# Optimization experiments

Measured on AMD Instinct MI355X. Metric: run time of the kernel, lower is better.

## Reference

```python
import jax, jax.numpy as jnp
import numpy as np

B, T, D = 4, 4096, 1024


def setup_inputs() -> dict:
    key = jax.random.key(0)
    ks = jax.random.split(key, 7)
    s_in = 1.0 / np.sqrt(D)
    return {
        "x": jax.random.normal(ks[0], (B, T, D), dtype=jnp.float32),
        "W_in": jax.random.uniform(ks[1], (D, 2 * D), jnp.float32, -s_in, s_in),
        "b_in": jax.random.uniform(ks[2], (2 * D,), jnp.float32, -s_in, s_in),
        "A": jax.random.normal(ks[3], (D,), dtype=jnp.float32),
        "C": jax.random.normal(ks[4], (D,), dtype=jnp.float32),
        "W_out": jax.random.uniform(ks[5], (D, D), jnp.float32, -s_in, s_in),
        "b_out": jax.random.uniform(ks[6], (D,), jnp.float32, -s_in, s_in),
    }


def _ssm(v, A, C):
    # diagonal linear recurrence: h_t = sigmoid(A) * h_{t-1} + v_t ; y_t = C * h_t
    decay = jax.nn.sigmoid(A)  # (D,)
    vT = jnp.swapaxes(v, 0, 1)  # (T, B, D)

    def step(h, vt):
        h = decay * h + vt
        return h, h

    h0 = jnp.zeros(vT.shape[1:], dtype=v.dtype)
    _, hs = jax.lax.scan(step, h0, vT)  # (T, B, D)
    return jnp.swapaxes(hs, 0, 1) * C  # (B, T, D)


def reference(x, W_in, b_in, A, C, W_out, b_out):
    proj = x @ W_in + b_in  # (B, T, 2D)
    v, gate = jnp.split(proj, 2, axis=-1)
    gate = jax.nn.sigmoid(gate)
    y = gate * _ssm(v, A, C)
    return y @ W_out + b_out
```

## Files before the change

kernel.cpp:

```cpp
#include <hip/hip_runtime.h>
#include <math.h>

#define BDIM 4
#define TDIM 4096
#define DDIM 1024
#define MDIM (BDIM * TDIM)

#define NC  64
#define LCH 64
static_assert(NC * LCH == TDIM, "chunking");

typedef __attribute__((ext_vector_type(8))) short short8;
typedef __attribute__((ext_vector_type(4))) float f32x4;

__device__ __forceinline__ unsigned short f2bf(float f) {
  unsigned int u = __float_as_uint(f);
  unsigned int r = (u + 0x7fffu + ((u >> 16) & 1u)) >> 16;
  return (unsigned short)r;
}
__device__ __forceinline__ float bf2f(unsigned short h) {
  return __uint_as_float(((unsigned int)h) << 16);
}
__device__ __forceinline__ float sigmoidf_(float x) {
  return 1.0f / (1.0f + expf(-x));
}

__global__ __launch_bounds__(256) void prep_x_kernel(const float* __restrict__ x,
                                                     unsigned short* __restrict__ xh,
                                                     int n4) {
  int i = blockIdx.x * 256 + threadIdx.x;
  if (i >= n4) return;
  float4 f = ((const float4*)x)[i];
  ushort4 h;
  h.x = f2bf(f.x);
  h.y = f2bf(f.y);
  h.z = f2bf(f.z);
  h.w = f2bf(f.w);
  ((ushort4*)xh)[i] = h;
}

__global__ __launch_bounds__(256) void wprep_kernel(const float* __restrict__ in,
                                                    unsigned short* __restrict__ oh,
                                                    int K, int N) {
  __shared__ float t[64][65];
  int n0 = blockIdx.x * 64;
  int k0 = blockIdx.y * 64;
#pragma unroll
  for (int i = 0; i < 16; ++i) {
    int idx = i * 256 + threadIdx.x;
    int r = idx >> 6, c = idx & 63;
    t[r][c] = in[(size_t)(k0 + r) * N + (n0 + c)];
  }
  __syncthreads();
#pragma unroll
  for (int i = 0; i < 16; ++i) {
    int idx = i * 256 + threadIdx.x;
    int rn = idx >> 6, ck = idx & 63;
    oh[(size_t)(n0 + rn) * K + (k0 + ck)] = f2bf(t[ck][rn]);
  }
}


__device__ __forceinline__ void stage_tile(unsigned short* ldsTile,
                                           const unsigned short* __restrict__ gTile,
                                           int ldK) {
  int wave = threadIdx.x >> 6;
  int lane = threadIdx.x & 63;
#pragma unroll
  for (int half = 0; half < 2; ++half) {
#pragma unroll
    for (int j = 0; j < 2; ++j) {
      int c = wave * 64 + lane + j * 512;
      int Lt = half * 16384 + c * 16;
      int P = Lt ^ (((Lt >> 7) & 7) << 4);
      const unsigned short* src = gTile + (size_t)(P >> 7) * ldK + ((P & 127) >> 1);
      unsigned short* dst = ldsTile + (half * 16384 + wave * 1024 + j * 8192) / 2;
      __builtin_amdgcn_global_load_lds(
          (const __attribute__((address_space(1))) unsigned int*)src,
          (__attribute__((address_space(3))) unsigned int*)dst, 16, 0, 0);
    }
  }
}

__device__ __forceinline__ short8 read_frag(const unsigned short* tile, int r, int kElem) {
  int addr = ((r << 7) + (kElem << 1)) ^ ((r & 7) << 4);
  return *(const short8*)((const char*)tile + addr);
}

#define BARRIER()                                  \
  do {                                             \
    asm volatile("" ::: "memory");                 \
    __builtin_amdgcn_s_barrier();                  \
    asm volatile("" ::: "memory");                 \
  } while (0)

#define READ_AF(SET, H, KKv)                                                    \
  _Pragma("unroll") for (int m = 0; m < 4; ++m)                                 \
      SET[m] = read_frag(As, rA + (H) * 64 + m * 16, (KKv) * 32 + kq);

#define READ_BF(KKv)                                                            \
  _Pragma("unroll") for (int n = 0; n < 4; ++n)                                 \
      bfr[n] = read_frag(Bs, rB + n * 16, (KKv) * 32 + kq);

#define MFMA16(SET, HH)                                                         \
  __builtin_amdgcn_s_setprio(1);                                                \
  _Pragma("unroll") for (int m = 0; m < 4; ++m)                                 \
      _Pragma("unroll") for (int n = 0; n < 4; ++n)                             \
          acc[(HH) * 4 + m][n] = __builtin_amdgcn_mfma_f32_16x16x32_bf16(       \
              SET[m], bfr[n], acc[(HH) * 4 + m][n], 0, 0, 0);                   \
  __builtin_amdgcn_s_setprio(0);

template <int EPI>
__global__ __launch_bounds__(512, 2) void gemm8p(const unsigned short* __restrict__ A,
                                                 const unsigned short* __restrict__ B,
                                                 const float* __restrict__ bias,
                                                 float* __restrict__ outF,
                                                 unsigned short* __restrict__ outV,
                                                 unsigned short* __restrict__ outG,
                                                 int nNt, int K) {
  __shared__ unsigned short ldsA[2 * 16384];
  __shared__ unsigned short ldsB[2 * 16384];

  int cpx = gridDim.x >> 3;
  int bid = blockIdx.x;
  int swz = (bid & 7) * cpx + (bid >> 3);
  int mtile = swz / nNt, ntile = swz % nNt;

  int wave = threadIdx.x >> 6, lane = threadIdx.x & 63;
  int wm = wave >> 2, wn = wave & 3;
  int rA = wm * 128 + (lane & 15);
  int rB = wn * 64 + (lane & 15);
  int kq = (lane >> 4) * 8;

  const unsigned short* Ag = A + (size_t)(mtile * 256) * K;
  const unsigned short* Bg = B + (size_t)(ntile * 256) * K;

  f32x4 acc[8][4] = {};
  short8 afA[4], afB[4], bfr[4];

  stage_tile(ldsA, Ag, K);
  stage_tile(ldsB, Bg, K);
  asm volatile("s_waitcnt vmcnt(0)" ::: "memory");
  BARRIER();

  int NT = K >> 6;
  for (int t = 0; t < NT; ++t) {
    const unsigned short* As = ldsA + (t & 1) * 16384;
    const unsigned short* Bs = ldsB + (t & 1) * 16384;
    unsigned short* An = ldsA + ((t + 1) & 1) * 16384;
    unsigned short* Bn = ldsB + ((t + 1) & 1) * 16384;
    bool pf = (t + 1 < NT);
    int k1 = (t + 1) << 6;

    READ_AF(afA, 0, 0);
    READ_BF(0);
    MFMA16(afA, 0);
    READ_AF(afB, 1, 0);
    if (pf) stage_tile(An, Ag + k1, K);
    BARRIER();
    MFMA16(afB, 1);
    READ_AF(afA, 0, 1);
    READ_BF(1);
    if (pf) stage_tile(Bn, Bg + k1, K);
    BARRIER();
    MFMA16(afA, 0);
    READ_AF(afB, 1, 1);
    BARRIER();
    MFMA16(afB, 1);
    if (pf) asm volatile("s_waitcnt vmcnt(0)" ::: "memory");
    BARRIER();
  }

  int row0 = mtile * 256 + wm * 128 + ((lane >> 4) << 2);
  int col0 = ntile * 256 + wn * 64 + (lane & 15);
#pragma unroll
  for (int m = 0; m < 8; ++m) {
#pragma unroll
    for (int n = 0; n < 4; ++n) {
      int col = col0 + n * 16;
      float bv = bias[col];
#pragma unroll
      for (int j = 0; j < 4; ++j) {
        int row = row0 + m * 16 + j;
        float val = acc[m][n][j] + bv;
        if (EPI == 0) {
          outF[(size_t)row * (nNt * 256) + col] = val;
        } else {
          if (col < DDIM)
            outV[(size_t)row * DDIM + col] = f2bf(val);
          else
            outG[(size_t)row * DDIM + (col - DDIM)] = f2bf(sigmoidf_(val));
        }
      }
    }
  }
}

__global__ __launch_bounds__(256) void ssm_phase1(const unsigned short* __restrict__ v,
                                                  const float* __restrict__ A,
                                                  float* __restrict__ chunkh) {
  int b = blockIdx.y, c = blockIdx.x;
  int d0 = threadIdx.x * 4;
  float4 a4 = *(const float4*)&A[d0];
  float dx = sigmoidf_(a4.x), dy = sigmoidf_(a4.y), dz = sigmoidf_(a4.z), dw = sigmoidf_(a4.w);
  float hx = 0.f, hy = 0.f, hz = 0.f, hw = 0.f;
  const ushort4* vp = (const ushort4*)(v + ((size_t)b * TDIM + (size_t)c * LCH) * DDIM + d0);
#pragma unroll 4
  for (int i = 0; i < LCH; ++i) {
    ushort4 vv = vp[(size_t)i * (DDIM / 4)];
    hx = fmaf(dx, hx, bf2f(vv.x));
    hy = fmaf(dy, hy, bf2f(vv.y));
    hz = fmaf(dz, hz, bf2f(vv.z));
    hw = fmaf(dw, hw, bf2f(vv.w));
  }
  float4 o = {hx, hy, hz, hw};
  *(float4*)&chunkh[(size_t)(b * NC + c) * DDIM + d0] = o;
}

__global__ __launch_bounds__(256) void ssm_phase2(const float* __restrict__ A,
                                                  float* __restrict__ chunkh) {
  int idx = blockIdx.x * 256 + threadIdx.x;
  int b = idx >> 10, d = idx & 1023;
  float dec = sigmoidf_(A[d]);
  float dL = dec;
#pragma unroll
  for (int i = 0; i < 6; ++i) dL *= dL;
  float hv[NC];
#pragma unroll
  for (int c = 0; c < NC; ++c) hv[c] = chunkh[(size_t)(b * NC + c) * DDIM + d];
  float carry = 0.f;
#pragma unroll
  for (int c = 0; c < NC; ++c) {
    float local = hv[c];
    hv[c] = carry;
    carry = fmaf(dL, carry, local);
  }
#pragma unroll
  for (int c = 0; c < NC; ++c) chunkh[(size_t)(b * NC + c) * DDIM + d] = hv[c];
}

__global__ __launch_bounds__(256) void ssm_phase3(const unsigned short* __restrict__ v,
                                                  const unsigned short* __restrict__ g,
                                                  const float* __restrict__ A,
                                                  const float* __restrict__ C,
                                                  const float* __restrict__ chunkh,
                                                  unsigned short* __restrict__ ybf) {
  int b = blockIdx.y, c = blockIdx.x;
  int d0 = threadIdx.x * 4;
  float4 a4 = *(const float4*)&A[d0];
  float4 c4 = *(const float4*)&C[d0];
  float dx = sigmoidf_(a4.x), dy = sigmoidf_(a4.y), dz = sigmoidf_(a4.z), dw = sigmoidf_(a4.w);
  float4 h0 = *(const float4*)&chunkh[(size_t)(b * NC + c) * DDIM + d0];
  float hx = h0.x, hy = h0.y, hz = h0.z, hw = h0.w;
  size_t base = ((size_t)b * TDIM + (size_t)c * LCH) * DDIM + d0;
  const ushort4* vp = (const ushort4*)(v + base);
  const ushort4* gp = (const ushort4*)(g + base);
  ushort4* yp = (ushort4*)(ybf + base);
#pragma unroll 4
  for (int i = 0; i < LCH; ++i) {
    ushort4 vv = vp[(size_t)i * (DDIM / 4)];
    ushort4 gg = gp[(size_t)i * (DDIM / 4)];
    hx = fmaf(dx, hx, bf2f(vv.x));
    hy = fmaf(dy, hy, bf2f(vv.y));
    hz = fmaf(dz, hz, bf2f(vv.z));
    hw = fmaf(dw, hw, bf2f(vv.w));
    ushort4 yy;
    yy.x = f2bf(bf2f(gg.x) * c4.x * hx);
    yy.y = f2bf(bf2f(gg.y) * c4.y * hy);
    yy.z = f2bf(bf2f(gg.z) * c4.z * hz);
    yy.w = f2bf(bf2f(gg.w) * c4.w * hw);
    yp[(size_t)i * (DDIM / 4)] = yy;
  }
}

extern "C" void kernel_launch(void* const* d_in, const int* in_sizes, int n_in,
                              void* d_out, int out_size, void* d_ws, size_t ws_size,
                              hipStream_t stream) {
  const float* x = (const float*)d_in[0];
  const float* W_in = (const float*)d_in[1];
  const float* b_in = (const float*)d_in[2];
  const float* A = (const float*)d_in[3];
  const float* C = (const float*)d_in[4];
  const float* W_out = (const float*)d_in[5];
  const float* b_out = (const float*)d_in[6];
  float* out = (float*)d_out;

  char* ws = (char*)d_ws;
  const size_t MK = (size_t)MDIM * DDIM;
  unsigned short* xh = (unsigned short*)ws;    ws += MK * 2;
  unsigned short* winh = (unsigned short*)ws;  ws += (size_t)2 * DDIM * DDIM * 2;
  unsigned short* wouth = (unsigned short*)ws; ws += (size_t)DDIM * DDIM * 2;
  unsigned short* v = (unsigned short*)ws;     ws += MK * 2;
  unsigned short* g = (unsigned short*)ws;     ws += MK * 2;
  unsigned short* ybf = (unsigned short*)ws;   ws += MK * 2;
  float* chunkh = (float*)ws;                  ws += (size_t)BDIM * NC * DDIM * 4;

  prep_x_kernel<<<(int)(MK / 4 / 256), 256, 0, stream>>>(x, xh, (int)(MK / 4));
  wprep_kernel<<<dim3(2 * DDIM / 64, DDIM / 64), 256, 0, stream>>>(W_in, winh, DDIM, 2 * DDIM);
  wprep_kernel<<<dim3(DDIM / 64, DDIM / 64), 256, 0, stream>>>(W_out, wouth, DDIM, DDIM);

  gemm8p<1><<<(MDIM / 256) * 8, 512, 0, stream>>>(xh, winh, b_in, nullptr, v, g, 8, DDIM);

  ssm_phase1<<<dim3(NC, BDIM), 256, 0, stream>>>(v, A, chunkh);
  ssm_phase2<<<(BDIM * DDIM) / 256, 256, 0, stream>>>(A, chunkh);
  ssm_phase3<<<dim3(NC, BDIM), 256, 0, stream>>>(v, g, A, C, chunkh, ybf);

  gemm8p<0><<<(MDIM / 256) * 4, 512, 0, stream>>>(ybf, wouth, b_out, out, nullptr, nullptr,
                                                  4, DDIM);
}
```

Baseline: 186.6 us.

## Restructure GEMM main loop with precomputed LDS offsets and single barrier per tile

Replaces the per-iteration address arithmetic for LDS fragment reads and global-to-LDS staging with base offsets computed once per thread. The loop is unrolled by two with compile-time buffer offsets, uses separate B fragment registers so loads of the second k-half can be issued while the first is consumed, and cuts the barriers per K-tile from four to one. The aim is to lower scalar/VALU overhead and barrier stalls in the MFMA loop, at the cost of more registers and a looser LDS write/read ordering that relies on the single trailing barrier.

```diff
diff --git a/kernel.cpp b/kernel.cpp
--- a/kernel.cpp
+++ b/kernel.cpp
@@ -61,32 +61,6 @@
 }
 
 
-__device__ __forceinline__ void stage_tile(unsigned short* ldsTile,
-                                           const unsigned short* __restrict__ gTile,
-                                           int ldK) {
-  int wave = threadIdx.x >> 6;
-  int lane = threadIdx.x & 63;
-#pragma unroll
-  for (int half = 0; half < 2; ++half) {
-#pragma unroll
-    for (int j = 0; j < 2; ++j) {
-      int c = wave * 64 + lane + j * 512;
-      int Lt = half * 16384 + c * 16;
-      int P = Lt ^ (((Lt >> 7) & 7) << 4);
-      const unsigned short* src = gTile + (size_t)(P >> 7) * ldK + ((P & 127) >> 1);
-      unsigned short* dst = ldsTile + (half * 16384 + wave * 1024 + j * 8192) / 2;
-      __builtin_amdgcn_global_load_lds(
-          (const __attribute__((address_space(1))) unsigned int*)src,
-          (__attribute__((address_space(3))) unsigned int*)dst, 16, 0, 0);
-    }
-  }
-}
-
-__device__ __forceinline__ short8 read_frag(const unsigned short* tile, int r, int kElem) {
-  int addr = ((r << 7) + (kElem << 1)) ^ ((r & 7) << 4);
-  return *(const short8*)((const char*)tile + addr);
-}
-
 #define BARRIER()                                  \
   do {                                             \
     asm volatile("" ::: "memory");                 \
@@ -94,21 +68,56 @@
     asm volatile("" ::: "memory");                 \
   } while (0)
 
-#define READ_AF(SET, H, KKv)                                                    \
+#define RD_A(SET, BUFC, H, BK)                                                  \
   _Pragma("unroll") for (int m = 0; m < 4; ++m)                                 \
-      SET[m] = read_frag(As, rA + (H) * 64 + m * 16, (KKv) * 32 + kq);
-
-#define READ_BF(KKv)                                                            \
+      SET[m] = *(const short8*)(ldsb + (((BK) ? baseA1 : baseA0) + (BUFC) +     \
+                                        (H) * 8192 + m * 2048));
+
+#define RD_B(SET, BUFC, BK)                                                     \
   _Pragma("unroll") for (int n = 0; n < 4; ++n)                                 \
-      bfr[n] = read_frag(Bs, rB + n * 16, (KKv) * 32 + kq);
-
-#define MFMA16(SET, HH)                                                         \
+      SET[n] = *(const short8*)(ldsbB + (((BK) ? baseB1 : baseB0) + (BUFC) +    \
+                                         n * 2048));
+
+#define MFMA16(ASET, BSET, HH)                                                  \
   __builtin_amdgcn_s_setprio(1);                                                \
   _Pragma("unroll") for (int m = 0; m < 4; ++m)                                 \
       _Pragma("unroll") for (int n = 0; n < 4; ++n)                             \
           acc[(HH) * 4 + m][n] = __builtin_amdgcn_mfma_f32_16x16x32_bf16(       \
-              SET[m], bfr[n], acc[(HH) * 4 + m][n], 0, 0, 0);                   \
+              ASET[m], BSET[n], acc[(HH) * 4 + m][n], 0, 0, 0);                 \
   __builtin_amdgcn_s_setprio(0);
+
+#define STAGE(PTR, S, BUFB, KOFF)                                               \
+  __builtin_amdgcn_global_load_lds(                                             \
+      (const __attribute__((address_space(1))) unsigned int*)((PTR) + off##S +  \
+                                                              (KOFF)),         \
+      (__attribute__((address_space(3))) unsigned int*)((char*)lds + (BUFB) +   \
+                                                        (S) * 8192 +            \
+                                                        wave * 1024),           \
+      16, 0, 0);
+
+#define TILE(T, BUFC, BUFN)                                                     \
+  {                                                                             \
+    bool pf = ((T) + 1 < NT);                                                   \
+    int k1 = ((T) + 1) << 7;          \
+    RD_A(afA, BUFC, 0, 0);                                                      \
+    RD_B(bfrA, BUFC, 0);                                                        \
+    if (pf) {                                                                   \
+      STAGE(AgB, 0, BUFN, k1) STAGE(AgB, 1, BUFN, k1)                           \
+      STAGE(AgB, 2, BUFN, k1) STAGE(AgB, 3, BUFN, k1)                           \
+    }                                                                           \
+    RD_A(afB, BUFC, 1, 0);                                                      \
+    MFMA16(afA, bfrA, 0);                                                       \
+    if (pf) { STAGE(BgB, 0, 65536 + (BUFN), k1) STAGE(BgB, 1, 65536 + (BUFN), k1) } \
+    RD_A(afA, BUFC, 0, 1);                                                      \
+    RD_B(bfrB, BUFC, 1);                                                        \
+    MFMA16(afB, bfrA, 1);                                                       \
+    if (pf) { STAGE(BgB, 2, 65536 + (BUFN), k1) STAGE(BgB, 3, 65536 + (BUFN), k1) } \
+    RD_A(afB, BUFC, 1, 1);                                                      \
+    MFMA16(afA, bfrB, 0);                                                       \
+    MFMA16(afB, bfrB, 1);                                                       \
+    if (pf) asm volatile("s_waitcnt vmcnt(0)" ::: "memory");                    \
+    BARRIER();                                                                  \
+  }
 
 template <int EPI>
 __global__ __launch_bounds__(512, 2) void gemm8p(const unsigned short* __restrict__ A,
@@ -118,57 +127,49 @@
                                                  unsigned short* __restrict__ outV,
                                                  unsigned short* __restrict__ outG,
                                                  int nNt, int K) {
-  __shared__ unsigned short ldsA[2 * 16384];
-  __shared__ unsigned short ldsB[2 * 16384];
+  __shared__ unsigned short lds[65536];
 
   int cpx = gridDim.x >> 3;
   int bid = blockIdx.x;
   int swz = (bid & 7) * cpx + (bid >> 3);
   int mtile = swz / nNt, ntile = swz % nNt;
 
-  int wave = threadIdx.x >> 6, lane = threadIdx.x & 63;
+  int tid = threadIdx.x;
+  int wave = tid >> 6, lane = tid & 63;
   int wm = wave >> 2, wn = wave & 3;
   int rA = wm * 128 + (lane & 15);
   int rB = wn * 64 + (lane & 15);
-  int kq = (lane >> 4) * 8;
-
-  const unsigned short* Ag = A + (size_t)(mtile * 256) * K;
-  const unsigned short* Bg = B + (size_t)(ntile * 256) * K;
+  int kq2 = (lane >> 4) * 16;
+
+  int baseA0 = ((rA << 7) + kq2) ^ ((rA & 7) << 4);
+  int baseA1 = ((rA << 7) + kq2 + 64) ^ ((rA & 7) << 4);
+  int baseB0 = ((rB << 7) + kq2) ^ ((rB & 7) << 4);
+  int baseB1 = ((rB << 7) + kq2 + 64) ^ ((rB & 7) << 4);
+  const char* ldsb = (const char*)lds;
+  const char* ldsbB = (const char*)lds + 65536;
+
+#define MKOFF(S) \
+  ({ int Lt = (S) * 8192 + tid * 16; int P = Lt ^ (((Lt >> 7) & 7) << 4); \
+     ((P >> 7) * (K << 1)) + (P & 127); })
+  int off0 = MKOFF(0), off1 = MKOFF(1), off2 = MKOFF(2), off3 = MKOFF(3);
+#undef MKOFF
+
+  const char* AgB = (const char*)(A + (size_t)(mtile * 256) * K);
+  const char* BgB = (const char*)(B + (size_t)(ntile * 256) * K);
 
   f32x4 acc[8][4] = {};
-  short8 afA[4], afB[4], bfr[4];
-
-  stage_tile(ldsA, Ag, K);
-  stage_tile(ldsB, Bg, K);
+  short8 afA[4], afB[4], bfrA[4], bfrB[4];
+
+  STAGE(AgB, 0, 0, 0) STAGE(AgB, 1, 0, 0) STAGE(AgB, 2, 0, 0) STAGE(AgB, 3, 0, 0)
+  STAGE(BgB, 0, 65536, 0) STAGE(BgB, 1, 65536, 0)
+  STAGE(BgB, 2, 65536, 0) STAGE(BgB, 3, 65536, 0)
   asm volatile("s_waitcnt vmcnt(0)" ::: "memory");
   BARRIER();
 
   int NT = K >> 6;
-  for (int t = 0; t < NT; ++t) {
-    const unsigned short* As = ldsA + (t & 1) * 16384;
-    const unsigned short* Bs = ldsB + (t & 1) * 16384;
-    unsigned short* An = ldsA + ((t + 1) & 1) * 16384;
-    unsigned short* Bn = ldsB + ((t + 1) & 1) * 16384;
-    bool pf = (t + 1 < NT);
-    int k1 = (t + 1) << 6;
-
-    READ_AF(afA, 0, 0);
-    READ_BF(0);
-    MFMA16(afA, 0);
-    READ_AF(afB, 1, 0);
-    if (pf) stage_tile(An, Ag + k1, K);
-    BARRIER();
-    MFMA16(afB, 1);
-    READ_AF(afA, 0, 1);
-    READ_BF(1);
-    if (pf) stage_tile(Bn, Bg + k1, K);
-    BARRIER();
-    MFMA16(afA, 0);
-    READ_AF(afB, 1, 1);
-    BARRIER();
-    MFMA16(afB, 1);
-    if (pf) asm volatile("s_waitcnt vmcnt(0)" ::: "memory");
-    BARRIER();
+  for (int t = 0; t < NT; t += 2) {
+    TILE(t, 0, 32768)
+    TILE(t + 1, 32768, 0)
   }
 
   int row0 = mtile * 256 + wm * 128 + ((lane >> 4) << 2);
```

Result: faster. 180.4 us (-3.3%).
